# Kernel tuning notes

Measured on AMD Instinct MI355X. Metric: run time of the kernel, lower is better.

Reference implementation:

```python
import jax, jax.numpy as jnp
import numpy as np

TAU = 1.5
MIN_TOKENS = 32
EPS = 1e-6


def setup_inputs() -> dict:
    key = jax.random.key(0)
    k1, k2 = jax.random.split(key)
    B, H, N, C = 4, 8, 2048, 512
    tokens = jax.random.normal(k1, (B, N, C), dtype=jnp.float32)
    # valid attention probabilities; sharpened logits so per-token entropy
    # straddles TAU and both the threshold and top-k branches are exercised
    logits = 10.0 * jax.random.normal(k2, (B, H, N, N), dtype=jnp.float32)
    attn_probs = jax.nn.softmax(logits, axis=-1)
    return {"tokens": tokens, "attn_probs": attn_probs}


def reference(tokens, attn_probs):
    # tokens: (B, N, C); attn_probs: (B, H, N, N)
    B, N, C = tokens.shape
    p = attn_probs.mean(axis=1)                              # (B, N, N) mean over heads
    entropy = -jnp.sum(p * jnp.log(p + EPS), axis=-1)        # (B, N)

    mask = entropy > TAU                                      # (B, N)
    count = jnp.sum(mask, axis=-1)                            # (B,) kept per batch

    # stable argsort on ~mask puts kept-token indices first, in original order
    compact_idx = jnp.argsort(~mask, axis=-1, stable=True)    # (B, N)

    # top-k fallback indices (sorted by entropy desc, like torch.topk)
    topk_idx = jax.lax.top_k(entropy, MIN_TOKENS)[1]          # (B, MIN_TOKENS)
    topk_pad = jnp.concatenate(
        [topk_idx, jnp.zeros((B, N - MIN_TOKENS), dtype=topk_idx.dtype)], axis=1)

    use_topk = count < MIN_TOKENS                             # (B,)
    idx = jnp.where(use_topk[:, None], topk_pad, compact_idx) # (B, N)
    keep_len = jnp.where(use_topk, MIN_TOKENS, count)         # (B,)

    gathered = jnp.take_along_axis(tokens, idx[:, :, None], axis=1)  # (B, N, C)
    valid = (jnp.arange(N)[None, :] < keep_len[:, None])             # (B, N)
    # zero-padded output; padded to N (static) instead of the data-dependent
    # max_len for jit compatibility — rows beyond max(keep_len) are all zero
    return gathered * valid[:, :, None].astype(tokens.dtype)
```

## Files before the change

### kernel.cpp

```cpp
#include <hip/hip_runtime.h>
#include <math.h>

constexpr int B = 4, H = 8, N = 2048, C = 512;
constexpr float TAU = 1.5f;
constexpr int MIN_TOKENS = 32;
constexpr float EPS = 1e-6f;

__global__ __launch_bounds__(256) void entropy_kernel(
    const float* __restrict__ attn, float* __restrict__ ent_out) {
    const int bi = blockIdx.x;
    const int b  = bi >> 11;
    const int i  = bi & (N - 1);
    const int t  = threadIdx.x;

    const float* base = attn + ((size_t)(b * H) * N + i) * (size_t)N;
    const size_t hstride = (size_t)N * N;

    float ent = 0.f;
#pragma unroll
    for (int iter = 0; iter < 2; ++iter) {
        const int j = iter * 1024 + t * 4;
        float4 s = make_float4(0.f, 0.f, 0.f, 0.f);
#pragma unroll
        for (int h = 0; h < H; ++h) {
            const float4 v =
                *reinterpret_cast<const float4*>(base + h * hstride + j);
            s.x += v.x; s.y += v.y; s.z += v.z; s.w += v.w;
        }
        float p;
        p = s.x * 0.125f; ent += p * logf(p + EPS);
        p = s.y * 0.125f; ent += p * logf(p + EPS);
        p = s.z * 0.125f; ent += p * logf(p + EPS);
        p = s.w * 0.125f; ent += p * logf(p + EPS);
    }

#pragma unroll
    for (int off = 32; off > 0; off >>= 1) ent += __shfl_down(ent, off, 64);
    __shared__ float ws[4];
    const int wid = t >> 6, lane = t & 63;
    if (lane == 0) ws[wid] = ent;
    __syncthreads();
    if (t == 0) ent_out[bi] = -(ws[0] + ws[1] + ws[2] + ws[3]);
}

__global__ __launch_bounds__(256) void select_kernel(
    const float* __restrict__ ent, int* __restrict__ idx_out,
    int* __restrict__ keep_out) {
    const int b = blockIdx.x;
    const int t = threadIdx.x;

    __shared__ float vals[N];
    __shared__ int   cnts[256];
    __shared__ float red_v[4];
    __shared__ int   red_i[4];

    for (int k = t; k < N; k += 256) vals[k] = ent[b * N + k];
    __syncthreads();

    int local = 0;
#pragma unroll
    for (int u = 0; u < 8; ++u) local += (vals[t * 8 + u] > TAU) ? 1 : 0;
    cnts[t] = local;
    __syncthreads();

    for (int off = 1; off < 256; off <<= 1) {
        const int v   = cnts[t];
        const int add = (t >= off) ? cnts[t - off] : 0;
        __syncthreads();
        cnts[t] = v + add;
        __syncthreads();
    }
    const int total = cnts[255];

    if (total >= MIN_TOKENS) {
        int pos = cnts[t] - local;
#pragma unroll
        for (int u = 0; u < 8; ++u) {
            const int k = t * 8 + u;
            if (vals[k] > TAU) idx_out[b * N + pos++] = k;
        }
        if (t == 0) keep_out[b] = total;
    } else {
        for (int k = 0; k < MIN_TOKENS; ++k) {
            float bv = -INFINITY; int bj = 0;
#pragma unroll
            for (int u = 0; u < 8; ++u) {
                const int j = t * 8 + u;
                const float v = vals[j];
                if (v > bv) { bv = v; bj = j; }
            }
#pragma unroll
            for (int off = 32; off > 0; off >>= 1) {
                const float ov = __shfl_down(bv, off, 64);
                const int   oj = __shfl_down(bj, off, 64);
                if (ov > bv || (ov == bv && oj < bj)) { bv = ov; bj = oj; }
            }
            const int wid = t >> 6, lane = t & 63;
            if (lane == 0) { red_v[wid] = bv; red_i[wid] = bj; }
            __syncthreads();
            if (t == 0) {
                float fv = red_v[0]; int fj = red_i[0];
#pragma unroll
                for (int w = 1; w < 4; ++w) {
                    if (red_v[w] > fv || (red_v[w] == fv && red_i[w] < fj)) {
                        fv = red_v[w]; fj = red_i[w];
                    }
                }
                idx_out[b * N + k] = fj;
                vals[fj] = -INFINITY;
            }
            __syncthreads();
        }
        if (t == 0) keep_out[b] = MIN_TOKENS;
    }
}

__global__ __launch_bounds__(128) void gather_kernel(
    const float* __restrict__ tokens, const int* __restrict__ idx,
    const int* __restrict__ keep, float* __restrict__ out) {
    const int br = blockIdx.x;
    const int b  = br >> 11;
    const int r  = br & (N - 1);
    const int t  = threadIdx.x;

    float4* orow = reinterpret_cast<float4*>(out + (size_t)br * C);
    if (r < keep[b]) {
        const int src = idx[br];
        const float4* srow = reinterpret_cast<const float4*>(
            tokens + ((size_t)b * N + src) * (size_t)C);
        orow[t] = srow[t];
    } else {
        orow[t] = make_float4(0.f, 0.f, 0.f, 0.f);
    }
}

extern "C" void kernel_launch(void* const* d_in, const int* in_sizes, int n_in,
                              void* d_out, int out_size, void* d_ws, size_t ws_size,
                              hipStream_t stream) {
    const float* tokens = (const float*)d_in[0];
    const float* attn   = (const float*)d_in[1];
    float* out = (float*)d_out;

    float* ent_ws  = (float*)d_ws;
    int*   idx_ws  = (int*)((char*)d_ws + (size_t)B * N * sizeof(float));
    int*   keep_ws = (int*)((char*)d_ws + 2 * (size_t)B * N * sizeof(float));

    entropy_kernel<<<B * N, 256, 0, stream>>>(attn, ent_ws);
    select_kernel<<<B, 256, 0, stream>>>(ent_ws, idx_ws, keep_ws);
    gather_kernel<<<B * N, 128, 0, stream>>>(tokens, idx_ws, keep_ws, out);
}
```

Baseline: 698.5 us.

## Batch all attention loads upfront and rewrite selection as per-wavefront register scan

```diff
diff --git a/kernel.cpp b/kernel.cpp
--- a/kernel.cpp
+++ b/kernel.cpp
@@ -16,16 +16,24 @@
     const float* base = attn + ((size_t)(b * H) * N + i) * (size_t)N;
     const size_t hstride = (size_t)N * N;
 
+    float4 v[2][8];
+#pragma unroll
+    for (int it = 0; it < 2; ++it) {
+        const int j = it * 1024 + t * 4;
+#pragma unroll
+        for (int h = 0; h < H; ++h) {
+            v[it][h] = *reinterpret_cast<const float4*>(base + h * hstride + j);
+        }
+    }
+
     float ent = 0.f;
 #pragma unroll
-    for (int iter = 0; iter < 2; ++iter) {
-        const int j = iter * 1024 + t * 4;
-        float4 s = make_float4(0.f, 0.f, 0.f, 0.f);
+    for (int it = 0; it < 2; ++it) {
+        float4 s = v[it][0];
 #pragma unroll
-        for (int h = 0; h < H; ++h) {
-            const float4 v =
-                *reinterpret_cast<const float4*>(base + h * hstride + j);
-            s.x += v.x; s.y += v.y; s.z += v.z; s.w += v.w;
+        for (int h = 1; h < H; ++h) {
+            s.x += v[it][h].x; s.y += v[it][h].y;
+            s.z += v[it][h].z; s.w += v[it][h].w;
         }
         float p;
         p = s.x * 0.125f; ent += p * logf(p + EPS);
@@ -46,72 +54,59 @@
 __global__ __launch_bounds__(256) void select_kernel(
     const float* __restrict__ ent, int* __restrict__ idx_out,
     int* __restrict__ keep_out) {
-    const int b = blockIdx.x;
     const int t = threadIdx.x;
+    const int b = t >> 6;
+    const int lane = t & 63;
 
-    __shared__ float vals[N];
-    __shared__ int   cnts[256];
-    __shared__ float red_v[4];
-    __shared__ int   red_i[4];
+    float v[32];
+#pragma unroll
+    for (int u = 0; u < 8; ++u) {
+        const float4 x = *reinterpret_cast<const float4*>(
+            ent + b * N + lane * 32 + u * 4);
+        v[u * 4 + 0] = x.x; v[u * 4 + 1] = x.y;
+        v[u * 4 + 2] = x.z; v[u * 4 + 3] = x.w;
+    }
 
-    for (int k = t; k < N; k += 256) vals[k] = ent[b * N + k];
-    __syncthreads();
+    int cnt = 0;
+#pragma unroll
+    for (int j = 0; j < 32; ++j) cnt += (v[j] > TAU) ? 1 : 0;
 
-    int local = 0;
+    int incl = cnt;
 #pragma unroll
-    for (int u = 0; u < 8; ++u) local += (vals[t * 8 + u] > TAU) ? 1 : 0;
-    cnts[t] = local;
-    __syncthreads();
-
-    for (int off = 1; off < 256; off <<= 1) {
-        const int v   = cnts[t];
-        const int add = (t >= off) ? cnts[t - off] : 0;
-        __syncthreads();
-        cnts[t] = v + add;
-        __syncthreads();
+    for (int off = 1; off < 64; off <<= 1) {
+        const int o = __shfl_up(incl, off, 64);
+        if (lane >= off) incl += o;
     }
-    const int total = cnts[255];
+    const int total = __shfl(incl, 63, 64);
+    const int excl = incl - cnt;
 
     if (total >= MIN_TOKENS) {
-        int pos = cnts[t] - local;
+        int pos = excl;
 #pragma unroll
-        for (int u = 0; u < 8; ++u) {
-            const int k = t * 8 + u;
-            if (vals[k] > TAU) idx_out[b * N + pos++] = k;
+        for (int j = 0; j < 32; ++j) {
+            if (v[j] > TAU) idx_out[b * N + pos++] = lane * 32 + j;
         }
-        if (t == 0) keep_out[b] = total;
+        if (lane == 0) keep_out[b] = total;
     } else {
         for (int k = 0; k < MIN_TOKENS; ++k) {
-            float bv = -INFINITY; int bj = 0;
+            float bv = -INFINITY; int bj = N;
 #pragma unroll
-            for (int u = 0; u < 8; ++u) {
-                const int j = t * 8 + u;
-                const float v = vals[j];
-                if (v > bv) { bv = v; bj = j; }
+            for (int j = 0; j < 32; ++j) {
+                if (v[j] > bv) { bv = v[j]; bj = lane * 32 + j; }
             }
 #pragma unroll
             for (int off = 32; off > 0; off >>= 1) {
-                const float ov = __shfl_down(bv, off, 64);
-                const int   oj = __shfl_down(bj, off, 64);
+                const float ov = __shfl_xor(bv, off, 64);
+                const int   oj = __shfl_xor(bj, off, 64);
                 if (ov > bv || (ov == bv && oj < bj)) { bv = ov; bj = oj; }
             }
-            const int wid = t >> 6, lane = t & 63;
-            if (lane == 0) { red_v[wid] = bv; red_i[wid] = bj; }
-            __syncthreads();
-            if (t == 0) {
-                float fv = red_v[0]; int fj = red_i[0];
+            if (lane == 0) idx_out[b * N + k] = bj;
 #pragma unroll
-                for (int w = 1; w < 4; ++w) {
-                    if (red_v[w] > fv || (red_v[w] == fv && red_i[w] < fj)) {
-                        fv = red_v[w]; fj = red_i[w];
-                    }
-                }
-                idx_out[b * N + k] = fj;
-                vals[fj] = -INFINITY;
+            for (int j = 0; j < 32; ++j) {
+                if (lane * 32 + j == bj) v[j] = -INFINITY;
             }
-            __syncthreads();
         }
-        if (t == 0) keep_out[b] = MIN_TOKENS;
+        if (lane == 0) keep_out[b] = MIN_TOKENS;
     }
 }
 
@@ -146,6 +141,6 @@
     int*   keep_ws = (int*)((char*)d_ws + 2 * (size_t)B * N * sizeof(float));
 
     entropy_kernel<<<B * N, 256, 0, stream>>>(attn, ent_ws);
-    select_kernel<<<B, 256, 0, stream>>>(ent_ws, idx_ws, keep_ws);
+    select_kernel<<<1, 256, 0, stream>>>(ent_ws, idx_ws, keep_ws);
     gather_kernel<<<B * N, 128, 0, stream>>>(tokens, idx_ws, keep_ws, out);
 }
```

After: 702.9 us. About the same (+0.6%).
